# Kernel tuning notes

Hardware: AMD Instinct MI355X
Metric: run time of the kernel (lower is better)

The kernel has to match this reference:

```python
import jax, jax.numpy as jnp
import numpy as np

INPUT_SIZE = 1024
HIDDEN_SIZE = 1024
LN_EPS = 1e-5


def setup_inputs() -> dict:
    key = jax.random.key(0)
    ks = jax.random.split(key, 8)
    bs, n = 4, 2048
    # Xavier-uniform bound for square (in=out) linear layers
    bound = float(np.sqrt(6.0 / (INPUT_SIZE + HIDDEN_SIZE)))
    x = jax.random.normal(ks[0], (bs, n, INPUT_SIZE), dtype=jnp.float32)
    wq = jax.random.uniform(ks[1], (INPUT_SIZE, HIDDEN_SIZE), jnp.float32, -bound, bound)
    wk = jax.random.uniform(ks[2], (INPUT_SIZE, HIDDEN_SIZE), jnp.float32, -bound, bound)
    wv = jax.random.uniform(ks[3], (INPUT_SIZE, HIDDEN_SIZE), jnp.float32, -bound, bound)
    bq = jnp.zeros((HIDDEN_SIZE,), jnp.float32)
    bk = jnp.zeros((HIDDEN_SIZE,), jnp.float32)
    bv = jnp.zeros((HIDDEN_SIZE,), jnp.float32)
    ln_w = jnp.ones((INPUT_SIZE,), jnp.float32)
    ln_b = jnp.zeros((INPUT_SIZE,), jnp.float32)
    return {"x": x, "wq": wq, "bq": bq, "wk": wk, "bk": bk,
            "wv": wv, "bv": bv, "ln_w": ln_w, "ln_b": ln_b}


def _layernorm(x, w, b):
    mu = jnp.mean(x, axis=-1, keepdims=True)
    var = jnp.mean(jnp.square(x - mu), axis=-1, keepdims=True)
    return (x - mu) * jax.lax.rsqrt(var + LN_EPS) * w + b


def reference(x, wq, bq, wk, bk, wv, bv, ln_w, ln_b):
    # x: [b, n, d_in]
    xn = _layernorm(x, ln_w, ln_b)
    q = jnp.einsum('bnd,dh->bnh', xn, wq) + bq
    k = jnp.einsum('bnd,dh->bnh', xn, wk) + bk
    v = jnp.einsum('bnd,dh->bnh', xn, wv) + bv
    scale = 1.0 / np.sqrt(HIDDEN_SIZE)
    att = jnp.einsum('bqh,bkh->bqk', q, k) * scale  # [b, n, n]
    att = jax.nn.softmax(att, axis=-1)
    out = jnp.einsum('bqk,bkh->bqh', att, v)  # [b, n, h]
    return (att, out)
```

## Files before the change

kernel.cpp:

```cpp
#include <hip/hip_runtime.h>
#include <stdint.h>


typedef __attribute__((ext_vector_type(8))) short short8;
typedef __attribute__((ext_vector_type(4))) float floatx4;
typedef __attribute__((ext_vector_type(4))) uint16_t u16x4;

__device__ __forceinline__ uint16_t f2bf(float f) {
    union { float f; uint32_t u; } v; v.f = f;
    uint32_t r = v.u + 0x7fffu + ((v.u >> 16) & 1u);
    return (uint16_t)(r >> 16);
}

typedef const uint32_t __attribute__((address_space(1)))* gas1_t;
typedef uint32_t __attribute__((address_space(3)))* las3_t;
__device__ __forceinline__ void gload_lds16(const uint16_t* g, uint16_t* l) {
    __builtin_amdgcn_global_load_lds((gas1_t)g, (las3_t)l, 16, 0, 0);
}

#define BM 128
#define BN 128
#define BKK 32

template<int EPI>
__device__ __forceinline__ void gemm_bt_body(
    const uint16_t* __restrict__ A, const uint16_t* __restrict__ Bt, int K,
    float* __restrict__ Cf, uint16_t* __restrict__ Cb, int ldc,
    const float* __restrict__ bias, float alpha)
{
    __shared__ uint16_t lA[BM * BKK];
    __shared__ uint16_t lB[BN * BKK];

    const int t  = threadIdx.x;
    const int m0 = blockIdx.y * BM;
    const int n0 = blockIdx.x * BN;

    const uint16_t* ga = A + (size_t)(m0 + (t >> 2)) * K + (t & 3) * 8;
    const uint16_t* gb = Bt + (size_t)(n0 + (t >> 2)) * K + (t & 3) * 8;
    uint16_t* la = &lA[t * 8];
    uint16_t* lb = &lB[t * 8];
    const size_t step64 = (size_t)64 * K;

    const int lane = t & 63;
    const int w    = t >> 6;
    const int quad = lane >> 4;
    const int lrow = lane & 15;
    const int wm   = (w & 1) * 64;
    const int wn   = (w >> 1) * 64;

    floatx4 acc[4][4];
#pragma unroll
    for (int i = 0; i < 4; i++)
#pragma unroll
        for (int j = 0; j < 4; j++)
            acc[i][j] = floatx4{0.f, 0.f, 0.f, 0.f};

    for (int k0 = 0; k0 < K; k0 += BKK) {
        __syncthreads();
        gload_lds16(ga + k0, la);
        gload_lds16(ga + step64 + k0, la + 2048);
        gload_lds16(gb + k0, lb);
        gload_lds16(gb + step64 + k0, lb + 2048);
        __syncthreads();

        short8 af[4], bf[4];
#pragma unroll
        for (int mi = 0; mi < 4; mi++)
            af[mi] = *(const short8*)&lA[(wm + mi * 16 + lrow) * BKK + quad * 8];
#pragma unroll
        for (int ni = 0; ni < 4; ni++)
            bf[ni] = *(const short8*)&lB[(wn + ni * 16 + lrow) * BKK + quad * 8];
#pragma unroll
        for (int mi = 0; mi < 4; mi++)
#pragma unroll
            for (int ni = 0; ni < 4; ni++)
                acc[mi][ni] = __builtin_amdgcn_mfma_f32_16x16x32_bf16(
                    af[mi], bf[ni], acc[mi][ni], 0, 0, 0);
    }

#pragma unroll
    for (int mi = 0; mi < 4; mi++) {
#pragma unroll
        for (int ni = 0; ni < 4; ni++) {
            const int row = m0 + wm + mi * 16 + quad * 4;
            const int col = n0 + wn + ni * 16 + lrow;
#pragma unroll
            for (int r = 0; r < 4; r++) {
                const float v = acc[mi][ni][r];
                if (EPI == 0) {
                    Cf[(size_t)(row + r) * ldc + col] = v * alpha;
                } else if (EPI == 1) {
                    Cb[(size_t)(row + r) * ldc + col] = f2bf(v + bias[col]);
                } else {
                    Cf[(size_t)(row + r) * ldc + col] = v;
                }
            }
        }
    }
}

__global__ __launch_bounds__(256) void k_qkv(
    const uint16_t* __restrict__ xn, const uint16_t* __restrict__ wt,
    const float* __restrict__ bq, const float* __restrict__ bk,
    const float* __restrict__ bv, uint16_t* __restrict__ qkv)
{
    const int z = blockIdx.z;
    const uint16_t* Bt = wt + (size_t)z * 1024 * 1024;
    const float* bias = (z == 0) ? bq : ((z == 1) ? bk : bv);
    uint16_t* C = qkv + (size_t)z * 8192 * 1024;
    gemm_bt_body<1>(xn, Bt, 1024, nullptr, C, 1024, bias, 0.f);
}

__global__ __launch_bounds__(256) void k_scores(
    const uint16_t* __restrict__ q, const uint16_t* __restrict__ k,
    float* __restrict__ S)
{
    const int z = blockIdx.z;
    gemm_bt_body<0>(q + (size_t)z * 2048 * 1024, k + (size_t)z * 2048 * 1024, 1024,
                    S + (size_t)z * 2048 * 2048, nullptr, 2048, nullptr, 0.03125f);
}

__global__ __launch_bounds__(256) void k_out(
    const uint16_t* __restrict__ attb, const uint16_t* __restrict__ vt,
    float* __restrict__ out)
{
    const int z = blockIdx.z;
    gemm_bt_body<2>(attb + (size_t)z * 2048 * 2048, vt + (size_t)z * 1024 * 2048, 2048,
                    out + (size_t)z * 2048 * 1024, nullptr, 1024, nullptr, 0.f);
}

__global__ __launch_bounds__(256) void k_ln(
    const float* __restrict__ x, const float* __restrict__ lw,
    const float* __restrict__ lb, uint16_t* __restrict__ xn)
{
    const int row = blockIdx.x;
    const int t = threadIdx.x;
    const float* xr = x + (size_t)row * 1024;
    const float4 xv = ((const float4*)xr)[t];
    float s  = xv.x + xv.y + xv.z + xv.w;
    float s2 = xv.x * xv.x + xv.y * xv.y + xv.z * xv.z + xv.w * xv.w;
#pragma unroll
    for (int off = 32; off > 0; off >>= 1) {
        s  += __shfl_xor(s, off);
        s2 += __shfl_xor(s2, off);
    }
    __shared__ float ps[4], ps2[4];
    const int w = t >> 6, lane = t & 63;
    if (lane == 0) { ps[w] = s; ps2[w] = s2; }
    __syncthreads();
    s  = ps[0] + ps[1] + ps[2] + ps[3];
    s2 = ps2[0] + ps2[1] + ps2[2] + ps2[3];
    const float mu  = s * (1.f / 1024.f);
    const float var = s2 * (1.f / 1024.f) - mu * mu;
    const float rs  = rsqrtf(var + 1e-5f);
    const float4 wv = ((const float4*)lw)[t];
    const float4 bv = ((const float4*)lb)[t];
    u16x4 o;
    o.x = f2bf((xv.x - mu) * rs * wv.x + bv.x);
    o.y = f2bf((xv.y - mu) * rs * wv.y + bv.y);
    o.z = f2bf((xv.z - mu) * rs * wv.z + bv.z);
    o.w = f2bf((xv.w - mu) * rs * wv.w + bv.w);
    ((u16x4*)(xn + (size_t)row * 1024))[t] = o;
}

__global__ void k_wt(const float* __restrict__ wq, const float* __restrict__ wk,
                     const float* __restrict__ wv, uint16_t* __restrict__ wt)
{
    __shared__ float tile[32][33];
    const int z = blockIdx.z;
    const float* W = (z == 0) ? wq : ((z == 1) ? wk : wv);
    uint16_t* T = wt + (size_t)z * 1024 * 1024;
    const int c0 = blockIdx.x * 32, r0 = blockIdx.y * 32;
    const int tx = threadIdx.x, ty = threadIdx.y;
#pragma unroll
    for (int i = 0; i < 4; i++)
        tile[ty + 8 * i][tx] = W[(size_t)(r0 + ty + 8 * i) * 1024 + c0 + tx];
    __syncthreads();
#pragma unroll
    for (int i = 0; i < 4; i++)
        T[(size_t)(c0 + ty + 8 * i) * 1024 + r0 + tx] = f2bf(tile[tx][ty + 8 * i]);
}

__global__ void k_vt(const uint16_t* __restrict__ v, uint16_t* __restrict__ vt)
{
    __shared__ uint16_t tile[32][33];
    const int b = blockIdx.z;
    const uint16_t* V = v + (size_t)b * 2048 * 1024;
    uint16_t* T = vt + (size_t)b * 2048 * 1024;
    const int c0 = blockIdx.x * 32, r0 = blockIdx.y * 32;
    const int tx = threadIdx.x, ty = threadIdx.y;
#pragma unroll
    for (int i = 0; i < 4; i++)
        tile[ty + 8 * i][tx] = V[(size_t)(r0 + ty + 8 * i) * 1024 + c0 + tx];
    __syncthreads();
#pragma unroll
    for (int i = 0; i < 4; i++)
        T[(size_t)(c0 + ty + 8 * i) * 2048 + r0 + tx] = tile[tx][ty + 8 * i];
}

__global__ __launch_bounds__(256) void k_softmax(
    float* __restrict__ S, uint16_t* __restrict__ attb)
{
    const size_t row = blockIdx.x;
    float* p = S + row * 2048;
    const int t = threadIdx.x;
    float4 a = ((float4*)p)[2 * t];
    float4 b = ((float4*)p)[2 * t + 1];
    float m = fmaxf(fmaxf(fmaxf(a.x, a.y), fmaxf(a.z, a.w)),
                    fmaxf(fmaxf(b.x, b.y), fmaxf(b.z, b.w)));
#pragma unroll
    for (int off = 32; off > 0; off >>= 1) m = fmaxf(m, __shfl_xor(m, off));
    __shared__ float pm[4], pl[4];
    const int w = t >> 6, lane = t & 63;
    if (lane == 0) pm[w] = m;
    __syncthreads();
    m = fmaxf(fmaxf(pm[0], pm[1]), fmaxf(pm[2], pm[3]));

    a.x = __expf(a.x - m); a.y = __expf(a.y - m);
    a.z = __expf(a.z - m); a.w = __expf(a.w - m);
    b.x = __expf(b.x - m); b.y = __expf(b.y - m);
    b.z = __expf(b.z - m); b.w = __expf(b.w - m);
    float s = a.x + a.y + a.z + a.w + b.x + b.y + b.z + b.w;
#pragma unroll
    for (int off = 32; off > 0; off >>= 1) s += __shfl_xor(s, off);
    if (lane == 0) pl[w] = s;
    __syncthreads();
    s = pl[0] + pl[1] + pl[2] + pl[3];
    const float inv = 1.f / s;

    a.x *= inv; a.y *= inv; a.z *= inv; a.w *= inv;
    b.x *= inv; b.y *= inv; b.z *= inv; b.w *= inv;
    ((float4*)p)[2 * t]     = a;
    ((float4*)p)[2 * t + 1] = b;

    uint16_t* q = attb + row * 2048 + t * 8;
    u16x4 o0, o1;
    o0.x = f2bf(a.x); o0.y = f2bf(a.y); o0.z = f2bf(a.z); o0.w = f2bf(a.w);
    o1.x = f2bf(b.x); o1.y = f2bf(b.y); o1.z = f2bf(b.z); o1.w = f2bf(b.w);
    ((u16x4*)q)[0] = o0;
    ((u16x4*)q)[1] = o1;
}

extern "C" void kernel_launch(void* const* d_in, const int* in_sizes, int n_in,
                              void* d_out, int out_size, void* d_ws, size_t ws_size,
                              hipStream_t stream)
{
    const float* x  = (const float*)d_in[0];
    const float* wq = (const float*)d_in[1];
    const float* bq = (const float*)d_in[2];
    const float* wk = (const float*)d_in[3];
    const float* bk = (const float*)d_in[4];
    const float* wv = (const float*)d_in[5];
    const float* bv = (const float*)d_in[6];
    const float* lw = (const float*)d_in[7];
    const float* lb = (const float*)d_in[8];

    float* att = (float*)d_out;
    float* out = (float*)d_out + (size_t)16777216;

    uint16_t* xn = (uint16_t*)d_out;
    uint16_t* wt = (uint16_t*)d_out + (size_t)8388608;

    uint16_t* ws   = (uint16_t*)d_ws;
    uint16_t* q    = ws;
    uint16_t* k    = ws + (size_t)8388608;
    uint16_t* v    = ws + (size_t)2 * 8388608;
    uint16_t* vt   = ws;
    uint16_t* attb = ws + (size_t)8388608;
    uint16_t* qkv  = q;

    if (ws_size < (size_t)50331648) return;

    k_ln<<<8192, 256, 0, stream>>>(x, lw, lb, xn);
    k_wt<<<dim3(32, 32, 3), dim3(32, 8), 0, stream>>>(wq, wk, wv, wt);
    k_qkv<<<dim3(8, 64, 3), 256, 0, stream>>>(xn, wt, bq, bk, bv, qkv);
    k_scores<<<dim3(16, 16, 4), 256, 0, stream>>>(q, k, att);
    k_vt<<<dim3(32, 64, 4), dim3(32, 8), 0, stream>>>(v, vt);
    k_softmax<<<8192, 256, 0, stream>>>(att, attb);
    k_out<<<dim3(8, 16, 4), 256, 0, stream>>>(attb, vt, out);
}
```

Before: 357.7 us.

## Double GEMM K-tile to 64 with XOR-swizzled LDS and vectorize V transpose

The shared bf16 GEMM body now stages 64-wide K tiles instead of 32, halving the number of sync/load iterations. The global-to-LDS loads use an XOR swizzle on the 16-byte segment index, and the fragment reads apply the matching swizzle to avoid LDS bank conflicts. The V transpose kernel switches to 64x64 tiles with 4-element vector loads and stores. Doubling LDS per block may lower occupancy.

```diff
diff --git a/kernel.cpp b/kernel.cpp
--- a/kernel.cpp
+++ b/kernel.cpp
@@ -20,7 +20,7 @@
 
 #define BM 128
 #define BN 128
-#define BKK 32
+#define BK2 64
 
 template<int EPI>
 __device__ __forceinline__ void gemm_bt_body(
@@ -28,18 +28,20 @@
     float* __restrict__ Cf, uint16_t* __restrict__ Cb, int ldc,
     const float* __restrict__ bias, float alpha)
 {
-    __shared__ uint16_t lA[BM * BKK];
-    __shared__ uint16_t lB[BN * BKK];
+    __shared__ uint16_t lA[BM * BK2];
+    __shared__ uint16_t lB[BN * BK2];
 
     const int t  = threadIdx.x;
     const int m0 = blockIdx.y * BM;
     const int n0 = blockIdx.x * BN;
 
-    const uint16_t* ga = A + (size_t)(m0 + (t >> 2)) * K + (t & 3) * 8;
-    const uint16_t* gb = Bt + (size_t)(n0 + (t >> 2)) * K + (t & 3) * 8;
+    const int srow = t >> 3;
+    const int sseg = (t & 7) ^ (srow & 7);
+    const uint16_t* ga = A + (size_t)(m0 + srow) * K + sseg * 8;
+    const uint16_t* gb = Bt + (size_t)(n0 + srow) * K + sseg * 8;
     uint16_t* la = &lA[t * 8];
     uint16_t* lb = &lB[t * 8];
-    const size_t step64 = (size_t)64 * K;
+    const size_t rstep = (size_t)32 * K;
 
     const int lane = t & 63;
     const int w    = t >> 6;
@@ -47,6 +49,7 @@
     const int lrow = lane & 15;
     const int wm   = (w & 1) * 64;
     const int wn   = (w >> 1) * 64;
+    const int swz  = lrow & 7;
 
     floatx4 acc[4][4];
 #pragma unroll
@@ -55,27 +58,36 @@
         for (int j = 0; j < 4; j++)
             acc[i][j] = floatx4{0.f, 0.f, 0.f, 0.f};
 
-    for (int k0 = 0; k0 < K; k0 += BKK) {
+    for (int k0 = 0; k0 < K; k0 += BK2) {
         __syncthreads();
-        gload_lds16(ga + k0, la);
-        gload_lds16(ga + step64 + k0, la + 2048);
-        gload_lds16(gb + k0, lb);
-        gload_lds16(gb + step64 + k0, lb + 2048);
+        gload_lds16(ga + k0,             la);
+        gload_lds16(ga + rstep + k0,     la + 2048);
+        gload_lds16(ga + 2 * rstep + k0, la + 4096);
+        gload_lds16(ga + 3 * rstep + k0, la + 6144);
+        gload_lds16(gb + k0,             lb);
+        gload_lds16(gb + rstep + k0,     lb + 2048);
+        gload_lds16(gb + 2 * rstep + k0, lb + 4096);
+        gload_lds16(gb + 3 * rstep + k0, lb + 6144);
         __syncthreads();
 
-        short8 af[4], bf[4];
-#pragma unroll
-        for (int mi = 0; mi < 4; mi++)
-            af[mi] = *(const short8*)&lA[(wm + mi * 16 + lrow) * BKK + quad * 8];
-#pragma unroll
-        for (int ni = 0; ni < 4; ni++)
-            bf[ni] = *(const short8*)&lB[(wn + ni * 16 + lrow) * BKK + quad * 8];
-#pragma unroll
-        for (int mi = 0; mi < 4; mi++)
+#pragma unroll
+        for (int ks = 0; ks < 2; ks++) {
+            short8 af[4], bf[4];
+#pragma unroll
+            for (int mi = 0; mi < 4; mi++)
+                af[mi] = *(const short8*)&lA[(wm + mi * 16 + lrow) * BK2 +
+                                             (((ks * 4 + quad) ^ swz) * 8)];
 #pragma unroll
             for (int ni = 0; ni < 4; ni++)
-                acc[mi][ni] = __builtin_amdgcn_mfma_f32_16x16x32_bf16(
-                    af[mi], bf[ni], acc[mi][ni], 0, 0, 0);
+                bf[ni] = *(const short8*)&lB[(wn + ni * 16 + lrow) * BK2 +
+                                             (((ks * 4 + quad) ^ swz) * 8)];
+#pragma unroll
+            for (int mi = 0; mi < 4; mi++)
+#pragma unroll
+                for (int ni = 0; ni < 4; ni++)
+                    acc[mi][ni] = __builtin_amdgcn_mfma_f32_16x16x32_bf16(
+                        af[mi], bf[ni], acc[mi][ni], 0, 0, 0);
+        }
     }
 
 #pragma unroll
@@ -181,21 +193,34 @@
         T[(size_t)(c0 + ty + 8 * i) * 1024 + r0 + tx] = f2bf(tile[tx][ty + 8 * i]);
 }
 
-__global__ void k_vt(const uint16_t* __restrict__ v, uint16_t* __restrict__ vt)
-{
-    __shared__ uint16_t tile[32][33];
+__global__ __launch_bounds__(256) void k_vt(
+    const uint16_t* __restrict__ v, uint16_t* __restrict__ vt)
+{
+    __shared__ uint16_t tile[64][68];
     const int b = blockIdx.z;
     const uint16_t* V = v + (size_t)b * 2048 * 1024;
-    uint16_t* T = vt + (size_t)b * 2048 * 1024;
-    const int c0 = blockIdx.x * 32, r0 = blockIdx.y * 32;
-    const int tx = threadIdx.x, ty = threadIdx.y;
-#pragma unroll
-    for (int i = 0; i < 4; i++)
-        tile[ty + 8 * i][tx] = V[(size_t)(r0 + ty + 8 * i) * 1024 + c0 + tx];
-    __syncthreads();
-#pragma unroll
-    for (int i = 0; i < 4; i++)
-        T[(size_t)(c0 + ty + 8 * i) * 2048 + r0 + tx] = tile[tx][ty + 8 * i];
+    uint16_t* T = vt + (size_t)b * 1024 * 2048;
+    const int h0 = blockIdx.x * 64, t0 = blockIdx.y * 64;
+    const int t = threadIdx.x;
+    const int rr = t >> 4;
+    const int cc = (t & 15) * 4;
+#pragma unroll
+    for (int i = 0; i < 4; i++) {
+        const int tok = rr + 16 * i;
+        *(u16x4*)&tile[tok][cc] =
+            *(const u16x4*)&V[(size_t)(t0 + tok) * 1024 + h0 + cc];
+    }
+    __syncthreads();
+#pragma unroll
+    for (int i = 0; i < 4; i++) {
+        const int h = rr + 16 * i;
+        u16x4 o;
+        o.x = tile[cc + 0][h];
+        o.y = tile[cc + 1][h];
+        o.z = tile[cc + 2][h];
+        o.w = tile[cc + 3][h];
+        *(u16x4*)&T[(size_t)(h0 + h) * 2048 + t0 + cc] = o;
+    }
 }
 
 __global__ __launch_bounds__(256) void k_softmax(
@@ -275,7 +300,7 @@
     k_wt<<<dim3(32, 32, 3), dim3(32, 8), 0, stream>>>(wq, wk, wv, wt);
     k_qkv<<<dim3(8, 64, 3), 256, 0, stream>>>(xn, wt, bq, bk, bv, qkv);
     k_scores<<<dim3(16, 16, 4), 256, 0, stream>>>(q, k, att);
-    k_vt<<<dim3(32, 64, 4), dim3(32, 8), 0, stream>>>(v, vt);
+    k_vt<<<dim3(16, 32, 4), 256, 0, stream>>>(v, vt);
     k_softmax<<<8192, 256, 0, stream>>>(att, attb);
     k_out<<<dim3(8, 16, 4), 256, 0, stream>>>(attb, vt, out);
 }
```

New measurement: 338.0 us. 5.5% less time.
